# Performance work log

Hardware: AMD Instinct MI355X
Metric: run time of the kernel (lower is better)

Reference implementation:

```python
import jax, jax.numpy as jnp
import numpy as np

LAM = 0.5


def _conv3x3(z, W):
    # z: [n, 2, h, w], W: [1, 2, 3, 3] (OIHW), padding=1, no bias
    return jax.lax.conv_general_dilated(
        z, W, window_strides=(1, 1), padding='SAME',
        dimension_numbers=('NCHW', 'OIHW', 'NCHW'))


def setup_inputs() -> dict:
    key = jax.random.key(0)
    k0, k1, k2, k3 = jax.random.split(key, 4)
    n, t, c, h, w = 32, 8, 128, 32, 32
    x = jax.random.normal(k0, (n, t, c, h, w), dtype=jnp.float32)
    alpha = jnp.full((1,), 0.5, dtype=jnp.float32)
    beta = jnp.full((1,), 0.5, dtype=jnp.float32)
    W_fc = jax.random.normal(k1, (t, t), dtype=jnp.float32) * (1.0 / np.sqrt(t))
    W_conv1 = jax.random.normal(k2, (1, 2, 3, 3), dtype=jnp.float32) * 0.2
    W_conv2 = jax.random.normal(k3, (1, 2, 3, 3), dtype=jnp.float32) * 0.2
    return {"x": x, "alpha": alpha, "beta": beta, "W_fc": W_fc,
            "W_conv1": W_conv1, "W_conv2": W_conv2}


def reference(x, alpha, beta, W_fc, W_conv1, W_conv2):
    n, t, c, h, w = x.shape
    # --- pooled time-channel map ---
    avg = jnp.mean(x, axis=(3, 4))            # [n,t,c]
    mx = jnp.max(x, axis=(3, 4))              # [n,t,c]
    map_add = 0.5 * (avg + mx) + alpha[0] * avg + beta[0] * mx
    # fc along time axis (Linear(t,t,bias=False) applied to [n,c,t]):
    # y[n,s,c] = sum_t map_add[n,t,c] * W_fc[s,t]
    map_add = jnp.einsum('ntc,st->nsc', map_add, W_fc)  # [n,t,c]

    kc = int(c * LAM)
    kt = int(t * LAM)
    # important channels: topk over channel axis, per timestep.
    # Faithful to the original: the fancy-index assignment unions the topk
    # selections over the batch, so the mask is batch-independent.
    _, idx_c = jax.lax.top_k(map_add, kc)                     # [n,t,kc]
    mask_c = jax.nn.one_hot(idx_c, c, dtype=x.dtype).max(axis=2).max(axis=0)  # [t,c]
    # important times: topk over time axis, per channel.
    _, idx_t = jax.lax.top_k(jnp.swapaxes(map_add, 1, 2), kt)  # [n,c,kt]
    mask_t = jax.nn.one_hot(idx_t, t, dtype=x.dtype).max(axis=2).max(axis=0).T  # [t,c]

    # torch.where((mask_c+mask_t)/2 == 0.5, 1, 0)  ==  XOR of the two masks
    im_tc = ((mask_c + mask_t) == 1.0).astype(x.dtype)  # [t,c]
    sub_tc = 1.0 - im_tc

    imf = x * im_tc[None, :, :, None, None]
    subf = x * sub_tc[None, :, :, None, None]
    imf = imf.reshape(n, t * c, h, w)
    subf = subf.reshape(n, t * c, h, w)

    im_avg = jnp.mean(imf, axis=1, keepdims=True) / LAM
    im_max = jnp.max(imf, axis=1, keepdims=True)
    sub_avg = jnp.mean(subf, axis=1, keepdims=True) / (1.0 - LAM)
    sub_max = jnp.max(subf, axis=1, keepdims=True)

    im_map = jax.nn.sigmoid(_conv3x3(jnp.concatenate([im_avg, im_max], axis=1), W_conv1))
    sub_map = jax.nn.sigmoid(_conv3x3(jnp.concatenate([sub_avg, sub_max], axis=1), W_conv2))

    out = im_map * imf + sub_map * subf                 # [n, t*c, h, w]
    return out.reshape(n, t, c, h, w)
```

## Files before the change

kernel.cpp:

```cpp
#include <hip/hip_runtime.h>
#include <math.h>

#define N_  32
#define TC  1024
#define P_  1024
#define KC  64
#define KT  4


__global__ void k0_zero(int* __restrict__ p) {
    int i = blockIdx.x * 256 + threadIdx.x;
    if (i < 2048) p[i] = 0;
}

__global__ __launch_bounds__(256) void k1_reduce(const float* __restrict__ x,
                                                 float* __restrict__ avg,
                                                 float* __restrict__ mx) {
    int r = blockIdx.x;
    const float4* xp = (const float4*)(x + (size_t)r * P_);
    float4 v = xp[threadIdx.x];
    float s = (v.x + v.y) + (v.z + v.w);
    float m = fmaxf(fmaxf(v.x, v.y), fmaxf(v.z, v.w));
    #pragma unroll
    for (int off = 32; off > 0; off >>= 1) {
        s += __shfl_down(s, off);
        m  = fmaxf(m, __shfl_down(m, off));
    }
    __shared__ float ss[4], sm[4];
    int wid = threadIdx.x >> 6, lane = threadIdx.x & 63;
    if (lane == 0) { ss[wid] = s; sm[wid] = m; }
    __syncthreads();
    if (threadIdx.x == 0) {
        float ts = (ss[0] + ss[1]) + (ss[2] + ss[3]);
        float tm = fmaxf(fmaxf(sm[0], sm[1]), fmaxf(sm[2], sm[3]));
        avg[r] = ts * (1.0f / 1024.0f);
        mx[r]  = tm;
    }
}

__global__ __launch_bounds__(256) void k2_map(const float* __restrict__ avg,
                                              const float* __restrict__ mx,
                                              const float* __restrict__ alpha,
                                              const float* __restrict__ beta,
                                              const float* __restrict__ wfc,
                                              int* __restrict__ mask_c,
                                              int* __restrict__ mask_t) {
    __shared__ float m[TC], mf[TC], w[64];
    int n = blockIdx.x;
    float a0 = alpha[0], b0 = beta[0];
    if (threadIdx.x < 64) w[threadIdx.x] = wfc[threadIdx.x];
    for (int i = threadIdx.x; i < TC; i += 256) {
        float a = avg[n * TC + i], b = mx[n * TC + i];
        m[i] = 0.5f * (a + b) + a0 * a + b0 * b;
    }
    __syncthreads();
    for (int i = threadIdx.x; i < TC; i += 256) {
        int s = i >> 7, cc = i & 127;
        float acc = 0.0f;
        #pragma unroll
        for (int tt = 0; tt < 8; ++tt) acc += m[tt * 128 + cc] * w[s * 8 + tt];
        mf[i] = acc;
    }
    __syncthreads();
    for (int i = threadIdx.x; i < TC; i += 256) {
        int tt = i >> 7, cc = i & 127;
        float v = mf[i];
        int rc = 0;
        for (int c2 = 0; c2 < 128; ++c2) {
            float u = mf[tt * 128 + c2];
            rc += (u > v) || (u == v && c2 < cc);
        }
        if (rc < KC) mask_c[i] = 1;
        int rt = 0;
        #pragma unroll
        for (int t2 = 0; t2 < 8; ++t2) {
            float u = mf[t2 * 128 + cc];
            rt += (u > v) || (u == v && t2 < tt);
        }
        if (rt < KT) mask_t[i] = 1;
    }
}

__global__ void k3_flag(const int* __restrict__ mc, const int* __restrict__ mt,
                        float* __restrict__ flag) {
    int i = blockIdx.x * 256 + threadIdx.x;
    if (i < TC) flag[i] = ((mc[i] != 0) != (mt[i] != 0)) ? 1.0f : 0.0f;
}

__global__ __launch_bounds__(1024) void k4_partial(const float* __restrict__ x,
                                                   const float* __restrict__ flag,
                                                   float* __restrict__ part) {
    __shared__ float sf[TC];
    sf[threadIdx.x] = flag[threadIdx.x];
    __syncthreads();
    int n = blockIdx.x >> 3, g = blockIdx.x & 7;
    const float* xb = x + (((size_t)n * TC + g * 128) * P_) + threadIdx.x;
    float ims = 0.0f, subs = 0.0f, imm = -INFINITY, subm = -INFINITY;
    for (int k = 0; k < 128; ++k) {
        float v = xb[(size_t)k * P_];
        bool im = sf[g * 128 + k] != 0.0f;
        float iv = im ? v : 0.0f;
        float sv = im ? 0.0f : v;
        ims += iv;  imm  = fmaxf(imm, iv);
        subs += sv; subm = fmaxf(subm, sv);
    }
    size_t base = (size_t)blockIdx.x * P_ + threadIdx.x;
    part[base]          = ims;
    part[base + 262144] = imm;
    part[base + 524288] = subs;
    part[base + 786432] = subm;
}

__global__ void k5_combine(const float* __restrict__ part,
                           float* __restrict__ pooled) {
    int id = blockIdx.x * 256 + threadIdx.x;
    int n = id >> 10, pix = id & 1023;
    float s_im = 0.0f, m_im = -INFINITY, s_sub = 0.0f, m_sub = -INFINITY;
    #pragma unroll
    for (int g = 0; g < 8; ++g) {
        size_t b = (size_t)(n * 8 + g) * P_ + pix;
        s_im  += part[b];
        m_im   = fmaxf(m_im, part[b + 262144]);
        s_sub += part[b + 524288];
        m_sub  = fmaxf(m_sub, part[b + 786432]);
    }
    float* pb = pooled + (size_t)n * 4 * P_;
    pb[0 * P_ + pix] = (s_im  / 1024.0f) / 0.5f;
    pb[1 * P_ + pix] = m_im;
    pb[2 * P_ + pix] = (s_sub / 1024.0f) / 0.5f;
    pb[3 * P_ + pix] = m_sub;
}

__global__ __launch_bounds__(1024) void k5_conv(const float* __restrict__ pooled,
                                                const float* __restrict__ w1,
                                                const float* __restrict__ w2,
                                                float* __restrict__ im_map,
                                                float* __restrict__ sub_map) {
    int n = blockIdx.x, pix = threadIdx.x;
    int y = pix >> 5, xx = pix & 31;
    const float* pb = pooled + (size_t)n * 4 * P_;
    float acc1 = 0.0f, acc2 = 0.0f;
    #pragma unroll
    for (int i = 0; i < 2; ++i)
        #pragma unroll
        for (int dy = 0; dy < 3; ++dy) {
            int yy = y + dy - 1;
            if (yy < 0 || yy >= 32) continue;
            #pragma unroll
            for (int dx = 0; dx < 3; ++dx) {
                int xc = xx + dx - 1;
                if (xc < 0 || xc >= 32) continue;
                acc1 += pb[i * P_ + yy * 32 + xc]       * w1[i * 9 + dy * 3 + dx];
                acc2 += pb[(2 + i) * P_ + yy * 32 + xc] * w2[i * 9 + dy * 3 + dx];
            }
        }
    im_map[n * P_ + pix]  = 1.0f / (1.0f + expf(-acc1));
    sub_map[n * P_ + pix] = 1.0f / (1.0f + expf(-acc2));
}

__global__ __launch_bounds__(256) void k6_out(const float* __restrict__ x,
                                              const float* __restrict__ flag,
                                              const float* __restrict__ im_map,
                                              const float* __restrict__ sub_map,
                                              float* __restrict__ out) {
    size_t i4 = (size_t)blockIdx.x * 256 + threadIdx.x;
    size_t e = i4 * 4;
    int n   = (int)(e >> 20);
    int rem = (int)(e & 1048575);
    int ch  = rem >> 10;
    int pix = rem & 1023;
    float4 xv = ((const float4*)x)[i4];
    bool im = flag[ch] != 0.0f;
    const float* mp = (im ? im_map : sub_map) + (size_t)n * P_ + pix;
    float4 mv = *(const float4*)mp;
    float4 o;
    o.x = xv.x * mv.x; o.y = xv.y * mv.y; o.z = xv.z * mv.z; o.w = xv.w * mv.w;
    ((float4*)out)[i4] = o;
}

extern "C" void kernel_launch(void* const* d_in, const int* in_sizes, int n_in,
                              void* d_out, int out_size, void* d_ws, size_t ws_size,
                              hipStream_t stream) {
    const float* x     = (const float*)d_in[0];
    const float* alpha = (const float*)d_in[1];
    const float* beta  = (const float*)d_in[2];
    const float* wfc   = (const float*)d_in[3];
    const float* w1    = (const float*)d_in[4];
    const float* w2    = (const float*)d_in[5];
    float* out = (float*)d_out;
    float* ws  = (float*)d_ws;

    float* avg     = ws;
    float* mx      = ws + 32768;
    int*   mask_c  = (int*)(ws + 65536);
    int*   mask_t  = (int*)(ws + 66560);
    float* flag    = ws + 67584;
    float* pooled  = ws + 68608;
    float* im_map  = ws + 199680;
    float* sub_map = ws + 232448;
    float* part    = ws + 265216;

    k0_zero   <<<8,     256, 0, stream>>>(mask_c);
    k1_reduce <<<32768, 256, 0, stream>>>(x, avg, mx);
    k2_map    <<<32,    256, 0, stream>>>(avg, mx, alpha, beta, wfc, mask_c, mask_t);
    k3_flag   <<<4,     256, 0, stream>>>(mask_c, mask_t, flag);
    k4_partial<<<256,  1024, 0, stream>>>(x, flag, part);
    k5_combine<<<128,   256, 0, stream>>>(part, pooled);
    k5_conv   <<<32,   1024, 0, stream>>>(pooled, w1, w2, im_map, sub_map);
    k6_out    <<<32768, 256, 0, stream>>>(x, flag, im_map, sub_map, out);
}
```

Baseline: 117.2 us.

## Fuse small kernels and widen partial channel reduction across more blocks

Folds the mask-zeroing kernel into the first reduce, the flag computation into the partial-reduction kernel, and the partial-combine step into the conv kernel, which cuts the launch count from eight to five. The partial reduction now runs 1024 blocks that each read float4 over 32 channels instead of 256 blocks over 128 channels, giving more parallelism and vectorised loads. Masking uses multiplication by the flag rather than selects. The price is a larger partial buffer and a 32-way combine inside each conv block.

Result: no change. 115.7 us (-1.2%).

```diff
diff --git a/kernel.cpp b/kernel.cpp
--- a/kernel.cpp
+++ b/kernel.cpp
@@ -1,22 +1,21 @@
 #include <hip/hip_runtime.h>
 #include <math.h>
 
-#define N_  32
 #define TC  1024
 #define P_  1024
 #define KC  64
 #define KT  4
 
 
-__global__ void k0_zero(int* __restrict__ p) {
-    int i = blockIdx.x * 256 + threadIdx.x;
-    if (i < 2048) p[i] = 0;
-}
-
 __global__ __launch_bounds__(256) void k1_reduce(const float* __restrict__ x,
                                                  float* __restrict__ avg,
-                                                 float* __restrict__ mx) {
+                                                 float* __restrict__ mx,
+                                                 int* __restrict__ masks) {
     int r = blockIdx.x;
+    if (r == 0) {
+        #pragma unroll
+        for (int j = 0; j < 8; ++j) masks[j * 256 + threadIdx.x] = 0;
+    }
     const float4* xp = (const float4*)(x + (size_t)r * P_);
     float4 v = xp[threadIdx.x];
     float s = (v.x + v.y) + (v.z + v.w);
@@ -66,6 +65,7 @@
         int tt = i >> 7, cc = i & 127;
         float v = mf[i];
         int rc = 0;
+        #pragma unroll 16
         for (int c2 = 0; c2 < 128; ++c2) {
             float u = mf[tt * 128 + c2];
             rc += (u > v) || (u == v && c2 < cc);
@@ -81,64 +81,70 @@
     }
 }
 
-__global__ void k3_flag(const int* __restrict__ mc, const int* __restrict__ mt,
-                        float* __restrict__ flag) {
-    int i = blockIdx.x * 256 + threadIdx.x;
-    if (i < TC) flag[i] = ((mc[i] != 0) != (mt[i] != 0)) ? 1.0f : 0.0f;
-}
-
-__global__ __launch_bounds__(1024) void k4_partial(const float* __restrict__ x,
-                                                   const float* __restrict__ flag,
-                                                   float* __restrict__ part) {
-    __shared__ float sf[TC];
-    sf[threadIdx.x] = flag[threadIdx.x];
-    __syncthreads();
-    int n = blockIdx.x >> 3, g = blockIdx.x & 7;
-    const float* xb = x + (((size_t)n * TC + g * 128) * P_) + threadIdx.x;
-    float ims = 0.0f, subs = 0.0f, imm = -INFINITY, subm = -INFINITY;
-    for (int k = 0; k < 128; ++k) {
-        float v = xb[(size_t)k * P_];
-        bool im = sf[g * 128 + k] != 0.0f;
-        float iv = im ? v : 0.0f;
-        float sv = im ? 0.0f : v;
-        ims += iv;  imm  = fmaxf(imm, iv);
-        subs += sv; subm = fmaxf(subm, sv);
-    }
-    size_t base = (size_t)blockIdx.x * P_ + threadIdx.x;
-    part[base]          = ims;
-    part[base + 262144] = imm;
-    part[base + 524288] = subs;
-    part[base + 786432] = subm;
-}
-
-__global__ void k5_combine(const float* __restrict__ part,
-                           float* __restrict__ pooled) {
-    int id = blockIdx.x * 256 + threadIdx.x;
-    int n = id >> 10, pix = id & 1023;
-    float s_im = 0.0f, m_im = -INFINITY, s_sub = 0.0f, m_sub = -INFINITY;
-    #pragma unroll
-    for (int g = 0; g < 8; ++g) {
-        size_t b = (size_t)(n * 8 + g) * P_ + pix;
-        s_im  += part[b];
-        m_im   = fmaxf(m_im, part[b + 262144]);
-        s_sub += part[b + 524288];
-        m_sub  = fmaxf(m_sub, part[b + 786432]);
-    }
-    float* pb = pooled + (size_t)n * 4 * P_;
-    pb[0 * P_ + pix] = (s_im  / 1024.0f) / 0.5f;
-    pb[1 * P_ + pix] = m_im;
-    pb[2 * P_ + pix] = (s_sub / 1024.0f) / 0.5f;
-    pb[3 * P_ + pix] = m_sub;
-}
-
-__global__ __launch_bounds__(1024) void k5_conv(const float* __restrict__ pooled,
+__global__ __launch_bounds__(256) void k4_partial(const float* __restrict__ x,
+                                                  const int* __restrict__ mask_c,
+                                                  const int* __restrict__ mask_t,
+                                                  float* __restrict__ flag_out,
+                                                  float* __restrict__ part) {
+    int b = blockIdx.x;
+    int kq = b & 3, g = (b >> 2) & 7, n = b >> 5;
+    __shared__ float sf[128];
+    if (threadIdx.x < 128) {
+        int ch = g * 128 + threadIdx.x;
+        float f = ((mask_c[ch] != 0) != (mask_t[ch] != 0)) ? 1.0f : 0.0f;
+        sf[threadIdx.x] = f;
+        if (n == 0 && kq == 0) flag_out[ch] = f;
+    }
+    __syncthreads();
+    const float4* xb = (const float4*)x
+                     + ((size_t)(n * TC + g * 128 + kq * 32) * 256) + threadIdx.x;
+    float4 ims  = {0.f, 0.f, 0.f, 0.f};
+    float4 subs = {0.f, 0.f, 0.f, 0.f};
+    float4 imm  = {-INFINITY, -INFINITY, -INFINITY, -INFINITY};
+    float4 subm = {-INFINITY, -INFINITY, -INFINITY, -INFINITY};
+    #pragma unroll 8
+    for (int k = 0; k < 32; ++k) {
+        float4 v = xb[(size_t)k * 256];
+        float f = sf[kq * 32 + k];
+        float iv;
+        iv = v.x * f; ims.x += iv; imm.x = fmaxf(imm.x, iv);
+        v.x -= iv;    subs.x += v.x; subm.x = fmaxf(subm.x, v.x);
+        iv = v.y * f; ims.y += iv; imm.y = fmaxf(imm.y, iv);
+        v.y -= iv;    subs.y += v.y; subm.y = fmaxf(subm.y, v.y);
+        iv = v.z * f; ims.z += iv; imm.z = fmaxf(imm.z, iv);
+        v.z -= iv;    subs.z += v.z; subm.z = fmaxf(subm.z, v.z);
+        iv = v.w * f; ims.w += iv; imm.w = fmaxf(imm.w, iv);
+        v.w -= iv;    subs.w += v.w; subm.w = fmaxf(subm.w, v.w);
+    }
+    float4* pp = (float4*)part + (size_t)b * 256 + threadIdx.x;
+    pp[0]      = ims;
+    pp[262144] = imm;
+    pp[524288] = subs;
+    pp[786432] = subm;
+}
+
+__global__ __launch_bounds__(1024) void k5_conv(const float* __restrict__ part,
                                                 const float* __restrict__ w1,
                                                 const float* __restrict__ w2,
                                                 float* __restrict__ im_map,
                                                 float* __restrict__ sub_map) {
-    int n = blockIdx.x, pix = threadIdx.x;
-    int y = pix >> 5, xx = pix & 31;
-    const float* pb = pooled + (size_t)n * 4 * P_;
+    __shared__ float sp[4][P_];
+    int n = blockIdx.x, p = threadIdx.x;
+    float s_im = 0.f, s_sub = 0.f, m_im = -INFINITY, m_sub = -INFINITY;
+    #pragma unroll 8
+    for (int gk = 0; gk < 32; ++gk) {
+        size_t idx = ((size_t)(n * 32 + gk)) * P_ + p;
+        s_im  += part[idx];
+        m_im   = fmaxf(m_im, part[idx + 1048576]);
+        s_sub += part[idx + 2097152];
+        m_sub  = fmaxf(m_sub, part[idx + 3145728]);
+    }
+    sp[0][p] = (s_im  * (1.0f / 1024.0f)) / 0.5f;
+    sp[1][p] = m_im;
+    sp[2][p] = (s_sub * (1.0f / 1024.0f)) / 0.5f;
+    sp[3][p] = m_sub;
+    __syncthreads();
+    int y = p >> 5, xx = p & 31;
     float acc1 = 0.0f, acc2 = 0.0f;
     #pragma unroll
     for (int i = 0; i < 2; ++i)
@@ -150,12 +156,12 @@
             for (int dx = 0; dx < 3; ++dx) {
                 int xc = xx + dx - 1;
                 if (xc < 0 || xc >= 32) continue;
-                acc1 += pb[i * P_ + yy * 32 + xc]       * w1[i * 9 + dy * 3 + dx];
-                acc2 += pb[(2 + i) * P_ + yy * 32 + xc] * w2[i * 9 + dy * 3 + dx];
+                acc1 += sp[i][yy * 32 + xc]     * w1[i * 9 + dy * 3 + dx];
+                acc2 += sp[2 + i][yy * 32 + xc] * w2[i * 9 + dy * 3 + dx];
             }
         }
-    im_map[n * P_ + pix]  = 1.0f / (1.0f + expf(-acc1));
-    sub_map[n * P_ + pix] = 1.0f / (1.0f + expf(-acc2));
+    im_map[n * P_ + p]  = 1.0f / (1.0f + expf(-acc1));
+    sub_map[n * P_ + p] = 1.0f / (1.0f + expf(-acc2));
 }
 
 __global__ __launch_bounds__(256) void k6_out(const float* __restrict__ x,
@@ -195,17 +201,13 @@
     int*   mask_c  = (int*)(ws + 65536);
     int*   mask_t  = (int*)(ws + 66560);
     float* flag    = ws + 67584;
-    float* pooled  = ws + 68608;
-    float* im_map  = ws + 199680;
-    float* sub_map = ws + 232448;
-    float* part    = ws + 265216;
-
-    k0_zero   <<<8,     256, 0, stream>>>(mask_c);
-    k1_reduce <<<32768, 256, 0, stream>>>(x, avg, mx);
+    float* im_map  = ws + 68608;
+    float* sub_map = ws + 101376;
+    float* part    = ws + 134144;
+
+    k1_reduce <<<32768, 256, 0, stream>>>(x, avg, mx, mask_c);
     k2_map    <<<32,    256, 0, stream>>>(avg, mx, alpha, beta, wfc, mask_c, mask_t);
-    k3_flag   <<<4,     256, 0, stream>>>(mask_c, mask_t, flag);
-    k4_partial<<<256,  1024, 0, stream>>>(x, flag, part);
-    k5_combine<<<128,   256, 0, stream>>>(part, pooled);
-    k5_conv   <<<32,   1024, 0, stream>>>(pooled, w1, w2, im_map, sub_map);
+    k4_partial<<<1024,  256, 0, stream>>>(x, mask_c, mask_t, flag, part);
+    k5_conv   <<<32,   1024, 0, stream>>>(part, w1, w2, im_map, sub_map);
     k6_out    <<<32768, 256, 0, stream>>>(x, flag, im_map, sub_map, out);
 }
```
